# Kernel tuning notes

Hardware: AMD Instinct MI355X
Metric: run time of the kernel (lower is better)

The kernel has to match this reference:

```python
import jax, jax.numpy as jnp
import numpy as np

SIZE_IN = 1024
SIZE_OUT = 1024
N_ROWS = 16384
MAX_VAL = 127.0  # nemo=False -> int8 path


def _quantize(t, max_val):
    """Per-tensor symmetric quantization matching the torch code.
    scale = max_val / max(|min(t)|, |max(t)|) (1.0 if t_max==0);
    q = clamp(round(scale*t), -max_val, max_val) cast to int8."""
    t_max = jnp.maximum(jnp.abs(jnp.min(t)), jnp.abs(jnp.max(t)))
    t_max = jnp.where(t_max == 0.0, 1.0, t_max)
    scale = max_val / t_max
    q = jnp.clip(jnp.round(scale * t), -max_val, max_val).astype(jnp.int8)
    return q, scale


def setup_inputs() -> dict:
    key = jax.random.key(0)
    kx, kw, kb = jax.random.split(key, 3)
    x = jax.random.normal(kx, (N_ROWS, SIZE_IN), dtype=jnp.float32)
    # kaiming_uniform_(a=sqrt(5)) -> uniform(-1/sqrt(fan_in), 1/sqrt(fan_in))
    bound = 1.0 / np.sqrt(SIZE_IN)
    weight = jax.random.uniform(kw, (SIZE_OUT, SIZE_IN), dtype=jnp.float32,
                                minval=-bound, maxval=bound)
    bias = jax.random.uniform(kb, (SIZE_OUT,), dtype=jnp.float32,
                              minval=-bound, maxval=bound)
    return {"x": x, "weight": weight, "bias": bias}


def reference(x, weight, bias):
    qw, sw = _quantize(weight, MAX_VAL)          # [SIZE_OUT, SIZE_IN] int8
    qx, sa = _quantize(x, MAX_VAL)               # [N, SIZE_IN] int8
    qb, sb = _quantize(bias, MAX_VAL)            # [SIZE_OUT] int8
    # for the approximate axx kernel), then dequantize.
    acc = jnp.matmul(qx.astype(jnp.int32), qw.astype(jnp.int32).T)  # [N, SIZE_OUT]
    out = acc.astype(jnp.float32) / (sa * sw)
    out = out + qb.astype(jnp.float32) / sb
    return out
```

## Files before the change

### kernel.cpp

```cpp
#include <hip/hip_runtime.h>


#define M_ROWS 16384
#define K_DIM  1024
#define N_OUT  1024

typedef int v4i __attribute__((ext_vector_type(4)));
typedef float v4f __attribute__((ext_vector_type(4)));

__device__ __forceinline__ void gload_lds16(const void* g, void* l) {
  __builtin_amdgcn_global_load_lds(
      (const __attribute__((address_space(1))) void*)g,
      (__attribute__((address_space(3))) void*)l, 16, 0, 0);
}

__device__ __forceinline__ float block_reduce_max4(float m, float* red) {
#pragma unroll
  for (int off = 32; off > 0; off >>= 1)
    m = fmaxf(m, __shfl_down(m, off));
  const int wid = threadIdx.x >> 6, lane = threadIdx.x & 63;
  if (lane == 0) red[wid] = m;
  __syncthreads();
  float r = fmaxf(fmaxf(red[0], red[1]), fmaxf(red[2], red[3]));
  __syncthreads();
  return r;
}

__global__ void amax_both(const float* __restrict__ x, const float* __restrict__ wsrc,
                          float* __restrict__ px, float* __restrict__ pw) {
  __shared__ float red[4];
  const bool isx = blockIdx.x < 2048;
  const float* src = isx ? x : wsrc;
  const int n4   = isx ? (M_ROWS * K_DIM / 4) : (N_OUT * K_DIM / 4);
  const int nblk = isx ? 2048 : 256;
  const int bidl = isx ? blockIdx.x : blockIdx.x - 2048;
  float m = 0.0f;
  const int stride = nblk * 256;
  for (int idx = bidl * 256 + threadIdx.x; idx < n4; idx += stride) {
    float4 v = ((const float4*)src)[idx];
    m = fmaxf(m, fmaxf(fmaxf(fabsf(v.x), fabsf(v.y)), fmaxf(fabsf(v.z), fabsf(v.w))));
  }
  float r = block_reduce_max4(m, red);
  if (threadIdx.x == 0) (isx ? px : pw)[bidl] = r;
}

__global__ void finalize_kernel(const float* __restrict__ px, int npx,
                                const float* __restrict__ pw, int npw,
                                const float* __restrict__ bias,
                                float* __restrict__ amax,
                                float* __restrict__ bdeq) {
  __shared__ float red[4];
  const int tid = threadIdx.x;

  float m = 0.0f;
  for (int i = tid; i < npx; i += 256) m = fmaxf(m, px[i]);
  float rx = block_reduce_max4(m, red);

  m = 0.0f;
  for (int i = tid; i < npw; i += 256) m = fmaxf(m, pw[i]);
  float rw = block_reduce_max4(m, red);

  float4 bv = ((const float4*)bias)[tid];
  m = fmaxf(fmaxf(fabsf(bv.x), fabsf(bv.y)), fmaxf(fabsf(bv.z), fabsf(bv.w)));
  float rb = block_reduce_max4(m, red);

  if (rx == 0.0f) rx = 1.0f;
  if (rw == 0.0f) rw = 1.0f;
  if (rb == 0.0f) rb = 1.0f;
  if (tid == 0) {
    amax[0] = rx;
    amax[1] = rw;
    amax[2] = rb;
  }
  const float sb = 127.0f / rb;
  float4 q;
  q.x = fminf(fmaxf(rintf(sb * bv.x), -127.0f), 127.0f) / sb;
  q.y = fminf(fmaxf(rintf(sb * bv.y), -127.0f), 127.0f) / sb;
  q.z = fminf(fmaxf(rintf(sb * bv.z), -127.0f), 127.0f) / sb;
  q.w = fminf(fmaxf(rintf(sb * bv.w), -127.0f), 127.0f) / sb;
  ((float4*)bdeq)[tid] = q;
}

__global__ void quant_both(const float* __restrict__ x, const float* __restrict__ wsrc,
                           signed char* __restrict__ qx, signed char* __restrict__ qw,
                           const float* __restrict__ amax) {
  const bool isx = blockIdx.x < 2048;
  const float* src = isx ? x : wsrc;
  signed char* dst = isx ? qx : qw;
  const int n4   = isx ? (M_ROWS * K_DIM / 4) : (N_OUT * K_DIM / 4);
  const int nblk = isx ? 2048 : 256;
  const int bidl = isx ? blockIdx.x : blockIdx.x - 2048;
  const float s = 127.0f / amax[isx ? 0 : 1];
  const int stride = nblk * 256;
  for (int idx = bidl * 256 + threadIdx.x; idx < n4; idx += stride) {
    float4 v = ((const float4*)src)[idx];
    int q0 = (int)fminf(fmaxf(rintf(s * v.x), -127.0f), 127.0f);
    int q1 = (int)fminf(fmaxf(rintf(s * v.y), -127.0f), 127.0f);
    int q2 = (int)fminf(fmaxf(rintf(s * v.z), -127.0f), 127.0f);
    int q3 = (int)fminf(fmaxf(rintf(s * v.w), -127.0f), 127.0f);
    unsigned int packed = (q0 & 0xff) | ((q1 & 0xff) << 8) |
                          ((q2 & 0xff) << 16) | ((q3 & 0xff) << 24);
    ((unsigned int*)dst)[idx] = packed;
  }
}

#define NKT 16

__global__ __launch_bounds__(512, 4) void gemm_kernel(
    const signed char* __restrict__ qx, const signed char* __restrict__ qw,
    const float* __restrict__ amax, const float* __restrict__ bdeq,
    float* __restrict__ out) {
  __shared__ char lds[49152];

  const int tid  = threadIdx.x;
  const int w    = tid >> 6;
  const int lane = tid & 63;
  const int wm = w >> 2;
  const int wn = w & 3;
  const int fr = lane & 15;
  const int q  = lane >> 4;

  const int bid = blockIdx.x;
  const int wg  = (bid & 7) * 128 + (bid >> 3);
  const int Mbase = (wg >> 3) * 128;
  const int Nbase = (wg & 7) * 128;

  const signed char* gA = qx + (size_t)Mbase * K_DIM;
  const signed char* gB = qw + (size_t)Nbase * K_DIM;

  const int scol = ((tid & 3) ^ ((tid >> 3) & 3)) << 4;
  const size_t srowK = (size_t)(tid >> 2) * K_DIM;
  const int u0 = (q ^ ((fr >> 1) & 3)) << 4;

  const float inv_denom = (amax[0] * amax[1]) * (1.0f / 16129.0f);

  v4i acc[4][2] = {};
  v4i Ar[4], Br[2];

#define STG(BASE, T)                                                           \
  do {                                                                         \
    const int _k0 = (T)*64 + scol;                                             \
    gload_lds16(gA + srowK + _k0, (BASE) + tid * 16);                          \
    gload_lds16(gB + srowK + _k0, (BASE) + 8192 + tid * 16);                   \
  } while (0)

#define VM(N) asm volatile("s_waitcnt vmcnt(" #N ")" ::: "memory")
#define LGKM0() asm volatile("s_waitcnt lgkmcnt(0)" ::: "memory")

  char* pR = lds;
  char* pS = lds + 16384;
  char* pF = lds + 32768;

  STG(pR, 0);

#pragma unroll
  for (int kt = 0; kt < NKT; ++kt) {
    if (kt + 1 < NKT) {
      STG(pS, kt + 1);
      VM(2);
    } else {
      VM(0);
    }
    __builtin_amdgcn_s_barrier();

    const char* _A = pR + wm * 4096;
    const char* _B = pR + 8192 + wn * 2048;
#pragma unroll
    for (int f = 0; f < 4; ++f)
      Ar[f] = *(const v4i*)(_A + f * 1024 + fr * 64 + u0);
#pragma unroll
    for (int g = 0; g < 2; ++g)
      Br[g] = *(const v4i*)(_B + g * 1024 + fr * 64 + u0);
#pragma unroll
    for (int f = 0; f < 4; ++f)
#pragma unroll
      for (int g = 0; g < 2; ++g)
        acc[f][g] = __builtin_amdgcn_mfma_i32_16x16x64_i8(Ar[f], Br[g], acc[f][g], 0, 0, 0);

    char* t = pR; pR = pS; pS = pF; pF = t;
  }
#undef STG

  __syncthreads();

  float bdq[2];
#pragma unroll
  for (int g = 0; g < 2; ++g) bdq[g] = bdeq[Nbase + wn * 32 + g * 16 + fr];

  float* lws = (float*)(lds + w * 4096);

  const int erow = lane >> 3;
  const int ecg  = lane & 7;
  float* const orow_base = out + (size_t)(Mbase + wm * 64) * N_OUT +
                           (Nbase + wn * 32) + ecg * 4;

#pragma unroll
  for (int f = 0; f < 4; ++f) {
#pragma unroll
    for (int g = 0; g < 2; ++g)
#pragma unroll
      for (int i = 0; i < 4; ++i)
        lws[(q * 4 + i) * 36 + g * 16 + fr] =
            (float)acc[f][g][i] * inv_denom + bdq[g];
    LGKM0();
#pragma unroll
    for (int t = 0; t < 2; ++t) {
      const int r16 = t * 8 + erow;
      v4f v = *(const v4f*)&lws[r16 * 36 + ecg * 4];
      __builtin_nontemporal_store(
          v, (v4f*)(orow_base + (size_t)(f * 16 + r16) * N_OUT));
    }
    LGKM0();
  }
#undef VM
#undef LGKM0
}

extern "C" void kernel_launch(void* const* d_in, const int* in_sizes, int n_in,
                              void* d_out, int out_size, void* d_ws, size_t ws_size,
                              hipStream_t stream) {
  const float* x = (const float*)d_in[0];
  const float* w = (const float*)d_in[1];
  const float* b = (const float*)d_in[2];
  float* out = (float*)d_out;

  char* ws = (char*)d_ws;
  float* amax = (float*)ws;
  float* bdeq = (float*)(ws + 256);
  float* px   = (float*)(ws + 8192);
  float* pw   = (float*)(ws + 16384 + 8192);
  signed char* qw = (signed char*)(ws + 65536);
  signed char* qx = (signed char*)(ws + (1 << 21));

  const int NPX = 2048, NPW = 256;
  hipLaunchKernelGGL(amax_both, dim3(NPX + NPW), dim3(256), 0, stream, x, w, px, pw);
  hipLaunchKernelGGL(finalize_kernel, dim3(1), dim3(256), 0, stream, px, NPX, pw, NPW, b, amax, bdeq);
  hipLaunchKernelGGL(quant_both, dim3(NPX + NPW), dim3(256), 0, stream, x, w, qx, qw, amax);
  hipLaunchKernelGGL(gemm_kernel, dim3(128 * 8), dim3(512), 0, stream, qx, qw, amax, bdeq, out);
}
```

Measured before the change: 58.97 us.

## Fuse amax, finalize and quantize into one cooperative kernel with grid sync

Replaces the three pre-GEMM kernels (partial amax, single-block finalize, quantize) with one cooperative kernel of 512 blocks. Each block does its partial max, a grid-wide sync follows, and then every block reduces the partials itself and quantizes its own slice. This removes two kernel launches and the serial single-block finalize step, and the second pass over x may hit in cache. In exchange it adds the cost of a cooperative launch and a grid barrier, and runs with fewer blocks than before.

```diff
diff --git a/kernel.cpp b/kernel.cpp
--- a/kernel.cpp
+++ b/kernel.cpp
@@ -1,4 +1,5 @@
 #include <hip/hip_runtime.h>
+#include <hip/hip_cooperative_groups.h>
 
 
 #define M_ROWS 16384
@@ -7,6 +8,8 @@
 
 typedef int v4i __attribute__((ext_vector_type(4)));
 typedef float v4f __attribute__((ext_vector_type(4)));
+
+namespace cg = cooperative_groups;
 
 __device__ __forceinline__ void gload_lds16(const void* g, void* l) {
   __builtin_amdgcn_global_load_lds(
@@ -26,73 +29,61 @@
   return r;
 }
 
-__global__ void amax_both(const float* __restrict__ x, const float* __restrict__ wsrc,
-                          float* __restrict__ px, float* __restrict__ pw) {
+#define NBX 448
+#define NBW 64
+
+__global__ void fused_pre(const float* __restrict__ x, const float* __restrict__ wsrc,
+                          const float* __restrict__ bias,
+                          signed char* __restrict__ qx, signed char* __restrict__ qw,
+                          float* __restrict__ px, float* __restrict__ pw,
+                          float* __restrict__ amax, float* __restrict__ bdeq) {
   __shared__ float red[4];
-  const bool isx = blockIdx.x < 2048;
-  const float* src = isx ? x : wsrc;
-  const int n4   = isx ? (M_ROWS * K_DIM / 4) : (N_OUT * K_DIM / 4);
-  const int nblk = isx ? 2048 : 256;
-  const int bidl = isx ? blockIdx.x : blockIdx.x - 2048;
-  float m = 0.0f;
-  const int stride = nblk * 256;
-  for (int idx = bidl * 256 + threadIdx.x; idx < n4; idx += stride) {
-    float4 v = ((const float4*)src)[idx];
-    m = fmaxf(m, fmaxf(fmaxf(fabsf(v.x), fabsf(v.y)), fmaxf(fabsf(v.z), fabsf(v.w))));
-  }
-  float r = block_reduce_max4(m, red);
-  if (threadIdx.x == 0) (isx ? px : pw)[bidl] = r;
-}
-
-__global__ void finalize_kernel(const float* __restrict__ px, int npx,
-                                const float* __restrict__ pw, int npw,
-                                const float* __restrict__ bias,
-                                float* __restrict__ amax,
-                                float* __restrict__ bdeq) {
-  __shared__ float red[4];
+  cg::grid_group grid = cg::this_grid();
+
   const int tid = threadIdx.x;
-
-  float m = 0.0f;
-  for (int i = tid; i < npx; i += 256) m = fmaxf(m, px[i]);
-  float rx = block_reduce_max4(m, red);
-
-  m = 0.0f;
-  for (int i = tid; i < npw; i += 256) m = fmaxf(m, pw[i]);
-  float rw = block_reduce_max4(m, red);
-
-  float4 bv = ((const float4*)bias)[tid];
-  m = fmaxf(fmaxf(fabsf(bv.x), fabsf(bv.y)), fmaxf(fabsf(bv.z), fabsf(bv.w)));
-  float rb = block_reduce_max4(m, red);
-
-  if (rx == 0.0f) rx = 1.0f;
-  if (rw == 0.0f) rw = 1.0f;
-  if (rb == 0.0f) rb = 1.0f;
-  if (tid == 0) {
-    amax[0] = rx;
-    amax[1] = rw;
-    amax[2] = rb;
-  }
-  const float sb = 127.0f / rb;
-  float4 q;
-  q.x = fminf(fmaxf(rintf(sb * bv.x), -127.0f), 127.0f) / sb;
-  q.y = fminf(fmaxf(rintf(sb * bv.y), -127.0f), 127.0f) / sb;
-  q.z = fminf(fmaxf(rintf(sb * bv.z), -127.0f), 127.0f) / sb;
-  q.w = fminf(fmaxf(rintf(sb * bv.w), -127.0f), 127.0f) / sb;
-  ((float4*)bdeq)[tid] = q;
-}
-
-__global__ void quant_both(const float* __restrict__ x, const float* __restrict__ wsrc,
-                           signed char* __restrict__ qx, signed char* __restrict__ qw,
-                           const float* __restrict__ amax) {
-  const bool isx = blockIdx.x < 2048;
+  const bool isx = blockIdx.x < NBX;
   const float* src = isx ? x : wsrc;
   signed char* dst = isx ? qx : qw;
   const int n4   = isx ? (M_ROWS * K_DIM / 4) : (N_OUT * K_DIM / 4);
-  const int nblk = isx ? 2048 : 256;
-  const int bidl = isx ? blockIdx.x : blockIdx.x - 2048;
-  const float s = 127.0f / amax[isx ? 0 : 1];
+  const int nblk = isx ? NBX : NBW;
+  const int bidl = isx ? blockIdx.x : blockIdx.x - NBX;
   const int stride = nblk * 256;
-  for (int idx = bidl * 256 + threadIdx.x; idx < n4; idx += stride) {
+
+  float m = 0.0f;
+  for (int idx = bidl * 256 + tid; idx < n4; idx += stride) {
+    float4 v = ((const float4*)src)[idx];
+    m = fmaxf(m, fmaxf(fmaxf(fabsf(v.x), fabsf(v.y)), fmaxf(fabsf(v.z), fabsf(v.w))));
+  }
+  float r = block_reduce_max4(m, red);
+  if (tid == 0) (isx ? px : pw)[bidl] = r;
+  __threadfence();
+  grid.sync();
+
+  m = 0.0f;
+  for (int i = tid; i < NBX; i += 256) m = fmaxf(m, px[i]);
+  float rx = block_reduce_max4(m, red);
+  m = (tid < NBW) ? pw[tid] : 0.0f;
+  float rw = block_reduce_max4(m, red);
+  if (rx == 0.0f) rx = 1.0f;
+  if (rw == 0.0f) rw = 1.0f;
+
+  if (blockIdx.x == 0) {
+    float4 bv = ((const float4*)bias)[tid];
+    m = fmaxf(fmaxf(fabsf(bv.x), fabsf(bv.y)), fmaxf(fabsf(bv.z), fabsf(bv.w)));
+    float rb = block_reduce_max4(m, red);
+    if (rb == 0.0f) rb = 1.0f;
+    if (tid == 0) { amax[0] = rx; amax[1] = rw; amax[2] = rb; }
+    const float sb = 127.0f / rb;
+    float4 qv;
+    qv.x = fminf(fmaxf(rintf(sb * bv.x), -127.0f), 127.0f) / sb;
+    qv.y = fminf(fmaxf(rintf(sb * bv.y), -127.0f), 127.0f) / sb;
+    qv.z = fminf(fmaxf(rintf(sb * bv.z), -127.0f), 127.0f) / sb;
+    qv.w = fminf(fmaxf(rintf(sb * bv.w), -127.0f), 127.0f) / sb;
+    ((float4*)bdeq)[tid] = qv;
+  }
+
+  const float s = 127.0f / (isx ? rx : rw);
+  for (int idx = bidl * 256 + tid; idx < n4; idx += stride) {
     float4 v = ((const float4*)src)[idx];
     int q0 = (int)fminf(fmaxf(rintf(s * v.x), -127.0f), 127.0f);
     int q1 = (int)fminf(fmaxf(rintf(s * v.y), -127.0f), 127.0f);
@@ -228,13 +219,13 @@
   float* amax = (float*)ws;
   float* bdeq = (float*)(ws + 256);
   float* px   = (float*)(ws + 8192);
-  float* pw   = (float*)(ws + 16384 + 8192);
+  float* pw   = (float*)(ws + 16384);
   signed char* qw = (signed char*)(ws + 65536);
   signed char* qx = (signed char*)(ws + (1 << 21));
 
-  const int NPX = 2048, NPW = 256;
-  hipLaunchKernelGGL(amax_both, dim3(NPX + NPW), dim3(256), 0, stream, x, w, px, pw);
-  hipLaunchKernelGGL(finalize_kernel, dim3(1), dim3(256), 0, stream, px, NPX, pw, NPW, b, amax, bdeq);
-  hipLaunchKernelGGL(quant_both, dim3(NPX + NPW), dim3(256), 0, stream, x, w, qx, qw, amax);
+  void* args[] = {(void*)&x, (void*)&w, (void*)&b, (void*)&qx, (void*)&qw,
+                  (void*)&px, (void*)&pw, (void*)&amax, (void*)&bdeq};
+  hipLaunchCooperativeKernel((const void*)fused_pre, dim3(NBX + NBW), dim3(256),
+                             args, 0, stream);
   hipLaunchKernelGGL(gemm_kernel, dim3(128 * 8), dim3(512), 0, stream, qx, qw, amax, bdeq, out);
 }
```

Result: slower. 148.0 us (+150.9%).

## Load GEMM B operand directly into registers, keep only A in LDS

Applied to the files above, without the earlier changes.

The int8 GEMM stops staging the weight (B) tile through LDS. Each wave now loads its B fragments straight from global memory into registers, double-buffered across pairs of K-steps, while A still goes through a triple-buffered LDS pipeline. This halves LDS traffic and footprint (48KB down to 24KB), which can raise occupancy and remove LDS reads for B. The trade-off is redundant global/L2 loads of B across the waves that share it, plus more registers and a hand-tuned vmcnt schedule that is easy to get wrong. The epilogue scratch stride shrinks to 3072 bytes per wave to fit the smaller buffer.

```diff
diff --git a/kernel.cpp b/kernel.cpp
--- a/kernel.cpp
+++ b/kernel.cpp
@@ -110,7 +110,7 @@
     const signed char* __restrict__ qx, const signed char* __restrict__ qw,
     const float* __restrict__ amax, const float* __restrict__ bdeq,
     float* __restrict__ out) {
-  __shared__ char lds[49152];
+  __shared__ char lds[24576];
 
   const int tid  = threadIdx.x;
   const int w    = tid >> 6;
@@ -126,60 +126,91 @@
   const int Nbase = (wg & 7) * 128;
 
   const signed char* gA = qx + (size_t)Mbase * K_DIM;
-  const signed char* gB = qw + (size_t)Nbase * K_DIM;
+  const signed char* pb0 = qw + (size_t)(Nbase + wn * 32 + fr) * K_DIM + q * 16;
+  const signed char* pb1 = pb0 + (size_t)16 * K_DIM;
 
   const int scol = ((tid & 3) ^ ((tid >> 3) & 3)) << 4;
   const size_t srowK = (size_t)(tid >> 2) * K_DIM;
-  const int u0 = (q ^ ((fr >> 1) & 3)) << 4;
+  const int aoff = (wm * 64 + fr) * 64 + ((q ^ ((fr >> 1) & 3)) << 4);
 
   const float inv_denom = (amax[0] * amax[1]) * (1.0f / 16129.0f);
 
   v4i acc[4][2] = {};
-  v4i Ar[4], Br[2];
+  v4i Ar[4];
+  v4i Ba[4], Bb[4];
 
 #define STG(BASE, T)                                                           \
-  do {                                                                         \
-    const int _k0 = (T)*64 + scol;                                             \
-    gload_lds16(gA + srowK + _k0, (BASE) + tid * 16);                          \
-    gload_lds16(gB + srowK + _k0, (BASE) + 8192 + tid * 16);                   \
-  } while (0)
+  gload_lds16(gA + srowK + (T)*64 + scol, (BASE) + tid * 16)
 
 #define VM(N) asm volatile("s_waitcnt vmcnt(" #N ")" ::: "memory")
 #define LGKM0() asm volatile("s_waitcnt lgkmcnt(0)" ::: "memory")
 
+#define RD_A()                                                                 \
+  do {                                                                         \
+    _Pragma("unroll") for (int f = 0; f < 4; ++f)                              \
+        Ar[f] = *(const v4i*)(pR + aoff + f * 1024);                           \
+  } while (0)
+
+#define MFMA2(B0v, B1v)                                                        \
+  do {                                                                         \
+    _Pragma("unroll") for (int f = 0; f < 4; ++f) {                            \
+      acc[f][0] = __builtin_amdgcn_mfma_i32_16x16x64_i8(Ar[f], (B0v), acc[f][0], 0, 0, 0); \
+      acc[f][1] = __builtin_amdgcn_mfma_i32_16x16x64_i8(Ar[f], (B1v), acc[f][1], 0, 0, 0); \
+    }                                                                          \
+  } while (0)
+
+#define LOADB(SET, J2)                                                         \
+  do {                                                                         \
+    SET[0] = *(const v4i*)(pb0 + (J2)*64);                                     \
+    SET[1] = *(const v4i*)(pb1 + (J2)*64);                                     \
+    SET[2] = *(const v4i*)(pb0 + (J2 + 1) * 64);                               \
+    SET[3] = *(const v4i*)(pb1 + (J2 + 1) * 64);                               \
+  } while (0)
+
+#define ROT() do { char* _t = pR; pR = pS; pS = pF; pF = _t; } while (0)
+
+#define PAIR(J, BCUR, BNXT, LAST)                                              \
+  do {                                                                         \
+                                                             \
+    STG(pS, 2 * (J) + 1);                                                      \
+    VM(1);                                                                     \
+    __builtin_amdgcn_s_barrier();                                              \
+    if (!(LAST)) LOADB(BNXT, 2 * (J) + 2);                                     \
+    RD_A();                                                                    \
+    MFMA2(BCUR[0], BCUR[1]);                                                   \
+    ROT();                                                                     \
+                                                            \
+    if (!(LAST)) { STG(pS, 2 * (J) + 2); VM(5); } else { VM(0); }              \
+    __builtin_amdgcn_s_barrier();                                              \
+    RD_A();                                                                    \
+    MFMA2(BCUR[2], BCUR[3]);                                                   \
+    ROT();                                                                     \
+  } while (0)
+
   char* pR = lds;
-  char* pS = lds + 16384;
-  char* pF = lds + 32768;
+  char* pS = lds + 8192;
+  char* pF = lds + 16384;
 
   STG(pR, 0);
-
-#pragma unroll
-  for (int kt = 0; kt < NKT; ++kt) {
-    if (kt + 1 < NKT) {
-      STG(pS, kt + 1);
-      VM(2);
-    } else {
-      VM(0);
-    }
-    __builtin_amdgcn_s_barrier();
-
-    const char* _A = pR + wm * 4096;
-    const char* _B = pR + 8192 + wn * 2048;
-#pragma unroll
-    for (int f = 0; f < 4; ++f)
-      Ar[f] = *(const v4i*)(_A + f * 1024 + fr * 64 + u0);
-#pragma unroll
-    for (int g = 0; g < 2; ++g)
-      Br[g] = *(const v4i*)(_B + g * 1024 + fr * 64 + u0);
-#pragma unroll
-    for (int f = 0; f < 4; ++f)
-#pragma unroll
-      for (int g = 0; g < 2; ++g)
-        acc[f][g] = __builtin_amdgcn_mfma_i32_16x16x64_i8(Ar[f], Br[g], acc[f][g], 0, 0, 0);
-
-    char* t = pR; pR = pS; pS = pF; pF = t;
-  }
+  LOADB(Ba, 0);
+  VM(0);
+  __builtin_amdgcn_s_barrier();
+
+  PAIR(0, Ba, Bb, 0);
+  PAIR(1, Bb, Ba, 0);
+  PAIR(2, Ba, Bb, 0);
+  PAIR(3, Bb, Ba, 0);
+  PAIR(4, Ba, Bb, 0);
+  PAIR(5, Bb, Ba, 0);
+  PAIR(6, Ba, Bb, 0);
+  PAIR(7, Bb, Ba, 1);
+
+#undef PAIR
+#undef LOADB
+#undef MFMA2
+#undef RD_A
 #undef STG
+#undef ROT
 
   __syncthreads();
 
@@ -187,7 +218,7 @@
 #pragma unroll
   for (int g = 0; g < 2; ++g) bdq[g] = bdeq[Nbase + wn * 32 + g * 16 + fr];
 
-  float* lws = (float*)(lds + w * 4096);
+  float* lws = (float*)(lds + w * 3072);
 
   const int erow = lane >> 3;
   const int ecg  = lane & 7;
```

New measurement: 74.57 us. +26.5%, slower.

## Preload the full A K-panel into LDS and double-buffer only B tiles

Applied to the files above, without the earlier changes.

The GEMM now loads the whole 128x1024 int8 A panel into LDS (128 KB) before the main loop. Only B tiles stream through a two-slot buffer, replacing the previous triple-buffered A+B pipeline. The aim is to cut per-iteration global load traffic and waiting on A. In exchange LDS use grows to 144 KB per block, which limits occupancy to one block per CU, and the full A load is exposed up front. Reducing to two B buffers with only one barrier per iteration also risks a write-after-read race on the buffer being refilled.

```diff
diff --git a/kernel.cpp b/kernel.cpp
--- a/kernel.cpp
+++ b/kernel.cpp
@@ -106,11 +106,11 @@
 
 #define NKT 16
 
-__global__ __launch_bounds__(512, 4) void gemm_kernel(
+__global__ __launch_bounds__(512, 2) void gemm_kernel(
     const signed char* __restrict__ qx, const signed char* __restrict__ qw,
     const float* __restrict__ amax, const float* __restrict__ bdeq,
     float* __restrict__ out) {
-  __shared__ char lds[49152];
+  __shared__ char lds[147456];
 
   const int tid  = threadIdx.x;
   const int w    = tid >> 6;
@@ -137,34 +137,34 @@
   v4i acc[4][2] = {};
   v4i Ar[4], Br[2];
 
-#define STG(BASE, T)                                                           \
-  do {                                                                         \
-    const int _k0 = (T)*64 + scol;                                             \
-    gload_lds16(gA + srowK + _k0, (BASE) + tid * 16);                          \
-    gload_lds16(gB + srowK + _k0, (BASE) + 8192 + tid * 16);                   \
-  } while (0)
+#define STG_B(BASE, T)                                                         \
+  gload_lds16(gB + srowK + (T)*64 + scol, (BASE) + tid * 16)
 
 #define VM(N) asm volatile("s_waitcnt vmcnt(" #N ")" ::: "memory")
 #define LGKM0() asm volatile("s_waitcnt lgkmcnt(0)" ::: "memory")
 
-  char* pR = lds;
-  char* pS = lds + 16384;
-  char* pF = lds + 32768;
-
-  STG(pR, 0);
+  char* pR = lds + 131072;
+  char* pS = lds + 131072 + 8192;
+
+#pragma unroll
+  for (int kt2 = 0; kt2 < NKT; ++kt2)
+    gload_lds16(gA + srowK + kt2 * 64 + scol, lds + kt2 * 8192 + tid * 16);
+  STG_B(pR, 0);
+  VM(0);
+  __builtin_amdgcn_s_barrier();
 
 #pragma unroll
   for (int kt = 0; kt < NKT; ++kt) {
     if (kt + 1 < NKT) {
-      STG(pS, kt + 1);
-      VM(2);
+      STG_B(pS, kt + 1);
+      VM(1);
     } else {
       VM(0);
     }
     __builtin_amdgcn_s_barrier();
 
-    const char* _A = pR + wm * 4096;
-    const char* _B = pR + 8192 + wn * 2048;
+    const char* _A = lds + kt * 8192 + wm * 4096;
+    const char* _B = pR + wn * 2048;
 #pragma unroll
     for (int f = 0; f < 4; ++f)
       Ar[f] = *(const v4i*)(_A + f * 1024 + fr * 64 + u0);
@@ -177,9 +177,9 @@
       for (int g = 0; g < 2; ++g)
         acc[f][g] = __builtin_amdgcn_mfma_i32_16x16x64_i8(Ar[f], Br[g], acc[f][g], 0, 0, 0);
 
-    char* t = pR; pR = pS; pS = pF; pF = t;
-  }
-#undef STG
+    char* t = pR; pR = pS; pS = t;
+  }
+#undef STG_B
 
   __syncthreads();
 
@@ -187,7 +187,7 @@
 #pragma unroll
   for (int g = 0; g < 2; ++g) bdq[g] = bdeq[Nbase + wn * 32 + g * 16 + fr];
 
-  float* lws = (float*)(lds + w * 4096);
+  float* lws = (float*)(lds + w * 3072);
 
   const int erow = lane >> 3;
   const int ecg  = lane & 7;
```

Result: slower. 64.56 us (+9.5%).
